# Kernel optimization log

Hardware: AMD Instinct MI355X
Metric: run time of the kernel (lower is better)

The kernel has to match this reference:

```python
import jax, jax.numpy as jnp
import numpy as np

N, E, IN, H, C = 50000, 800000, 128, 4, 32


def setup_inputs() -> dict:
    key = jax.random.key(0)
    ks = jax.random.split(key, 10)
    scale = 1.0 / np.sqrt(IN)
    x = jax.random.normal(ks[0], (N, IN), dtype=jnp.float32)
    edge_index = jax.random.randint(ks[1], (2, E), 0, N, dtype=jnp.int64)
    Wq = jax.random.uniform(ks[2], (IN, H * C), jnp.float32, -scale, scale)
    bq = jnp.zeros((H * C,), jnp.float32)
    Wk = jax.random.uniform(ks[3], (IN, H * C), jnp.float32, -scale, scale)
    bk = jnp.zeros((H * C,), jnp.float32)
    Wv = jax.random.uniform(ks[4], (IN, H * C), jnp.float32, -scale, scale)
    bv = jnp.zeros((H * C,), jnp.float32)
    Wskip = jax.random.uniform(ks[5], (IN, H * C), jnp.float32, -scale, scale)
    bskip = jnp.zeros((H * C,), jnp.float32)
    return {"x": x, "edge_index": edge_index, "Wq": Wq, "bq": bq,
            "Wk": Wk, "bk": bk, "Wv": Wv, "bv": bv,
            "Wskip": Wskip, "bskip": bskip}


def reference(x, edge_index, Wq, bq, Wk, bk, Wv, bv, Wskip, bskip):
    # PyG TransformerConv: edge messages flow src -> dst
    src, dst = edge_index[0], edge_index[1]
    q = (x @ Wq + bq).reshape(N, H, C)
    k = (x @ Wk + bk).reshape(N, H, C)
    v = (x @ Wv + bv).reshape(N, H, C)
    # per-edge attention logits [E, H]
    alpha = jnp.einsum('ehc,ehc->eh', q[dst], k[src]) / jnp.sqrt(jnp.float32(C))
    # scatter-softmax over incoming edges of each dst node
    m = jax.ops.segment_max(alpha, dst, num_segments=N)  # [N, H]
    ex = jnp.exp(alpha - m[dst])
    denom = jax.ops.segment_sum(ex, dst, num_segments=N)  # [N, H]
    w = ex / denom[dst]  # [E, H]
    # weighted scatter-add of values
    agg = jax.ops.segment_sum(v[src] * w[:, :, None], dst, num_segments=N)  # [N,H,C]
    out = agg.reshape(N, H * C) + x @ Wskip + bskip
    return out
```

## Files before the change

kernel.cpp:

```cpp
#include <hip/hip_runtime.h>
#include <hip/hip_bf16.h>

#define NNODES 50000
#define NEDGES 800000
#define FDIM   128
#define NHEADS 4
#define NSCANB ((NNODES + 1023) / 1024)

typedef __attribute__((ext_vector_type(8))) short  bf16x8;
typedef __attribute__((ext_vector_type(4))) float  f32x4;

static __device__ __forceinline__ unsigned short f2bf(float f) {
    __hip_bfloat16 h = __float2bfloat16(f);
    return *reinterpret_cast<unsigned short*>(&h);
}
static __device__ __forceinline__ float bf2f(unsigned short u) {
    return __uint_as_float(((unsigned int)u) << 16);
}

__global__ __launch_bounds__(256) void tgd_cvt_x(const float* __restrict__ x,
                                                 unsigned short* __restrict__ xb)
{
    size_t base = ((size_t)blockIdx.x * 256 + threadIdx.x) * 8;
    if (base >= (size_t)NNODES * FDIM) return;
    float4 f0 = *reinterpret_cast<const float4*>(&x[base]);
    float4 f1 = *reinterpret_cast<const float4*>(&x[base + 4]);
    unsigned short u[8];
    u[0]=f2bf(f0.x); u[1]=f2bf(f0.y); u[2]=f2bf(f0.z); u[3]=f2bf(f0.w);
    u[4]=f2bf(f1.x); u[5]=f2bf(f1.y); u[6]=f2bf(f1.z); u[7]=f2bf(f1.w);
    *reinterpret_cast<uint4*>(&xb[base]) = *reinterpret_cast<uint4*>(u);
}

__global__ __launch_bounds__(256) void tgd_cvt_w(
    const float* __restrict__ Wq, const float* __restrict__ Wk,
    const float* __restrict__ Wv, const float* __restrict__ Wsk,
    unsigned short* __restrict__ Wt2)
{
    int t = blockIdx.x * 256 + threadIdx.x;
    if (t >= 4 * 8 * 4 * 64) return;
    int m    = t >> 11;
    int ct   = (t >> 8) & 7;
    int ks   = (t >> 6) & 3;
    int lane = t & 63;
    int c  = ct * 16 + (lane & 15);
    int k0 = ks * 32 + (lane >> 4) * 8;
    const float* W = (m == 0) ? Wq : (m == 1) ? Wk : (m == 2) ? Wv : Wsk;
    unsigned short u[8];
    #pragma unroll
    for (int j = 0; j < 8; ++j)
        u[j] = f2bf(W[(size_t)(k0 + j) * FDIM + c]);
    *reinterpret_cast<uint4*>(&Wt2[(size_t)t * 8]) = *reinterpret_cast<uint4*>(u);
}

__global__ __launch_bounds__(512) void tgd_gemm_mfma(
    const unsigned short* __restrict__ xb, const unsigned short* __restrict__ Wt2,
    const float* __restrict__ bq, const float* __restrict__ bk,
    const float* __restrict__ bv, const float* __restrict__ bsk,
    float* __restrict__ q, unsigned short* __restrict__ kv,
    float* __restrict__ outp)
{
    const int tid  = threadIdx.x;
    const int wave = tid >> 6, lane = tid & 63;
    const int mp   = wave >> 2;
    const int wr   = wave & 3;
    const int r0   = blockIdx.x * 64 + wr * 16;
    const int l16  = lane & 15, lhi = lane >> 4;

    int arow = r0 + l16;
    int arow_c = (arow < NNODES) ? arow : (NNODES - 1);
    const unsigned short* abase = xb + (size_t)arow_c * FDIM + lhi * 8;
    bf16x8 a[4];
    #pragma unroll
    for (int ks = 0; ks < 4; ++ks)
        a[ks] = *reinterpret_cast<const bf16x8*>(abase + ks * 32);

    f32x4 acc[2][8];
    #pragma unroll
    for (int m2 = 0; m2 < 2; ++m2)
        #pragma unroll
        for (int ct = 0; ct < 8; ++ct)
            acc[m2][ct] = (f32x4){0.f, 0.f, 0.f, 0.f};

    #pragma unroll
    for (int ks = 0; ks < 4; ++ks) {
        #pragma unroll
        for (int m2 = 0; m2 < 2; ++m2) {
            const int m = mp * 2 + m2;
            const unsigned short* wb =
                Wt2 + ((size_t)(((m * 8 + 0) * 4 + ks) * 64) + lane) * 8;
            #pragma unroll
            for (int ct = 0; ct < 8; ++ct) {
                bf16x8 b = *reinterpret_cast<const bf16x8*>(wb + (size_t)ct * 4 * 64 * 8);
                acc[m2][ct] = __builtin_amdgcn_mfma_f32_16x16x32_bf16(
                    a[ks], b, acc[m2][ct], 0, 0, 0);
            }
        }
    }

    #pragma unroll
    for (int m2 = 0; m2 < 2; ++m2) {
        const int m = mp * 2 + m2;
        const float* bias = (m == 0) ? bq : (m == 1) ? bk : (m == 2) ? bv : bsk;
        #pragma unroll
        for (int ct = 0; ct < 8; ++ct) {
            int col = ct * 16 + l16;
            float bval = bias[col];
            #pragma unroll
            for (int r = 0; r < 4; ++r) {
                int row = r0 + lhi * 4 + r;
                if (row >= NNODES) continue;
                float val = acc[m2][ct][r] + bval;
                if (m == 0)       q[(size_t)row * FDIM + col] = val;
                else if (m == 3)  outp[(size_t)row * FDIM + col] = val;
                else              kv[(size_t)row * 256 + (m == 2 ? 128 : 0) + col] = f2bf(val);
            }
        }
    }
}

__global__ __launch_bounds__(256) void tgd_hist(const int* __restrict__ ei,
                                                int* __restrict__ deg)
{
    int t = blockIdx.x * 256 + threadIdx.x;
    if (t < NEDGES) atomicAdd(&deg[ei[NEDGES + t]], 1);
}

__global__ __launch_bounds__(1024) void tgd_scan1(const int* __restrict__ deg,
                                                  int* __restrict__ rowptr,
                                                  int* __restrict__ bsum)
{
    __shared__ int buf[1024];
    const int tid = threadIdx.x;
    const int i   = blockIdx.x * 1024 + tid;
    int d = (i < NNODES) ? deg[i] : 0;
    buf[tid] = d;
    __syncthreads();
    #pragma unroll
    for (int off = 1; off < 1024; off <<= 1) {
        int t2 = (tid >= off) ? buf[tid - off] : 0;
        __syncthreads();
        buf[tid] += t2;
        __syncthreads();
    }
    if (i < NNODES) rowptr[i + 1] = buf[tid];
    if (tid == 1023) bsum[blockIdx.x] = buf[1023];
}

__global__ __launch_bounds__(64) void tgd_scan2(const int* __restrict__ bsum,
                                                int* __restrict__ boff)
{
    int lane = threadIdx.x;
    int v = (lane < NSCANB) ? bsum[lane] : 0;
    int own = v;
    #pragma unroll
    for (int off = 1; off < 64; off <<= 1) {
        int t = __shfl_up(v, off);
        if (lane >= off) v += t;
    }
    if (lane < NSCANB) boff[lane] = v - own;
}

__global__ __launch_bounds__(1024) void tgd_scan3(const int* __restrict__ deg,
                                                  const int* __restrict__ boff,
                                                  int* __restrict__ rowptr,
                                                  int* __restrict__ ofs)
{
    const int i = blockIdx.x * 1024 + threadIdx.x;
    if (i < NNODES) {
        int r = rowptr[i + 1] + boff[blockIdx.x];
        rowptr[i + 1] = r;
        ofs[i] = r - deg[i];
    }
    if (i == 0) rowptr[0] = 0;
}

__global__ __launch_bounds__(256) void tgd_build(const int* __restrict__ ei,
                                                 int* __restrict__ ofs,
                                                 int* __restrict__ csr)
{
    int t = blockIdx.x * 256 + threadIdx.x;
    if (t >= NEDGES) return;
    int src = ei[t];
    int dst = ei[NEDGES + t];
    int pos = atomicAdd(&ofs[dst], 1);
    csr[pos] = src;
}

__global__ __launch_bounds__(256) void tgd_agg(
    const int* __restrict__ csr, const int* __restrict__ rowptr,
    const float* __restrict__ q, const unsigned short* __restrict__ kv,
    float* __restrict__ outp)
{
    const int node = blockIdx.x * 4 + (threadIdx.x >> 6);
    const int lane = threadIdx.x & 63;
    if (node >= NNODES) return;
    const int start = rowptr[node];
    const int end   = rowptr[node + 1];
    if (start == end) return;

    const bool isK = (lane < 32);
    float4 qv = {0.f, 0.f, 0.f, 0.f};
    if (isK) qv = *reinterpret_cast<const float4*>(&q[(size_t)node * FDIM + lane * 4]);
    const float inv = 0.17677669529663687f;

    float  den = 0.0f;
    float4 acc = {0.f, 0.f, 0.f, 0.f};

    for (int base = start; base < end; base += 64) {
        const int cnt = min(64, end - base);
        int myid = (lane < cnt) ? csr[base + lane] : 0;

        int j = 0;
        for (; j + 1 < cnt; j += 2) {
            int s0 = __shfl(myid, j);
            int s1 = __shfl(myid, j + 1);
            ushort4 r0 = *reinterpret_cast<const ushort4*>(&kv[(size_t)s0 * 256 + lane * 4]);
            ushort4 r1 = *reinterpret_cast<const ushort4*>(&kv[(size_t)s1 * 256 + lane * 4]);

            float a0 = bf2f(r0.x), a1 = bf2f(r0.y), a2 = bf2f(r0.z), a3 = bf2f(r0.w);
            float b0 = bf2f(r1.x), b1 = bf2f(r1.y), b2 = bf2f(r1.z), b3 = bf2f(r1.w);

            float sA = qv.x*a0 + qv.y*a1 + qv.z*a2 + qv.w*a3;
            float sB = qv.x*b0 + qv.y*b1 + qv.z*b2 + qv.w*b3;
            sA += __shfl_xor(sA, 1);  sB += __shfl_xor(sB, 1);
            sA += __shfl_xor(sA, 2);  sB += __shfl_xor(sB, 2);
            sA += __shfl_xor(sA, 4);  sB += __shfl_xor(sB, 4);
            float wA = __expf(sA * inv);
            float wB = __expf(sB * inv);
            wA = __shfl_xor(wA, 32);
            wB = __shfl_xor(wB, 32);
            if (!isK) {
                den += wA + wB;
                acc.x += wA*a0 + wB*b0;
                acc.y += wA*a1 + wB*b1;
                acc.z += wA*a2 + wB*b2;
                acc.w += wA*a3 + wB*b3;
            }
        }
        if (j < cnt) {
            int s0 = __shfl(myid, j);
            ushort4 r0 = *reinterpret_cast<const ushort4*>(&kv[(size_t)s0 * 256 + lane * 4]);
            float a0 = bf2f(r0.x), a1 = bf2f(r0.y), a2 = bf2f(r0.z), a3 = bf2f(r0.w);
            float sA = qv.x*a0 + qv.y*a1 + qv.z*a2 + qv.w*a3;
            sA += __shfl_xor(sA, 1);
            sA += __shfl_xor(sA, 2);
            sA += __shfl_xor(sA, 4);
            float wA = __expf(sA * inv);
            wA = __shfl_xor(wA, 32);
            if (!isK) {
                den += wA;
                acc.x += wA*a0; acc.y += wA*a1; acc.z += wA*a2; acc.w += wA*a3;
            }
        }
    }

    if (!isK) {
        float invd = 1.0f / den;
        float4* o = reinterpret_cast<float4*>(&outp[(size_t)node * FDIM + (lane - 32) * 4]);
        float4 cur = *o;
        cur.x += acc.x * invd;
        cur.y += acc.y * invd;
        cur.z += acc.z * invd;
        cur.w += acc.w * invd;
        *o = cur;
    }
}

extern "C" void kernel_launch(void* const* d_in, const int* in_sizes, int n_in,
                              void* d_out, int out_size, void* d_ws, size_t ws_size,
                              hipStream_t stream) {
    const float* x   = (const float*)d_in[0];
    const int*   ei  = (const int*)  d_in[1];
    const float* Wq  = (const float*)d_in[2];
    const float* bq  = (const float*)d_in[3];
    const float* Wk  = (const float*)d_in[4];
    const float* bk  = (const float*)d_in[5];
    const float* Wv  = (const float*)d_in[6];
    const float* bv  = (const float*)d_in[7];
    const float* Wsk = (const float*)d_in[8];
    const float* bsk = (const float*)d_in[9];
    float* outp = (float*)d_out;

    float* ws = (float*)d_ws;
    float*          q   = ws;
    unsigned short* kv  = (unsigned short*)(q + (size_t)NNODES * FDIM);
    unsigned short* xb  = kv + (size_t)NNODES * 256;
    unsigned short* Wt2 = xb + (size_t)NNODES * FDIM;
    int* deg    = (int*)(Wt2 + 4 * FDIM * FDIM);
    int* rowptr = deg + NNODES;
    int* ofs    = rowptr + NNODES + 1;
    int* csr    = ofs + NNODES;
    int* bsum   = csr + NEDGES;
    int* boff   = bsum + NSCANB;

    hipMemsetAsync(deg, 0, (size_t)NNODES * sizeof(int), stream);

    tgd_cvt_x<<<(NNODES * FDIM / 8 + 255) / 256, 256, 0, stream>>>(x, xb);
    tgd_cvt_w<<<(4 * 8 * 4 * 64 + 255) / 256, 256, 0, stream>>>(Wq, Wk, Wv, Wsk, Wt2);

    tgd_gemm_mfma<<<(NNODES + 63) / 64, 512, 0, stream>>>(
        xb, Wt2, bq, bk, bv, bsk, q, kv, outp);

    tgd_hist<<<(NEDGES + 255) / 256, 256, 0, stream>>>(ei, deg);
    tgd_scan1<<<NSCANB, 1024, 0, stream>>>(deg, rowptr, bsum);
    tgd_scan2<<<1, 64, 0, stream>>>(bsum, boff);
    tgd_scan3<<<NSCANB, 1024, 0, stream>>>(deg, boff, rowptr, ofs);
    tgd_build<<<(NEDGES + 255) / 256, 256, 0, stream>>>(ei, ofs, csr);
    tgd_agg<<<(NNODES + 3) / 4, 256, 0, stream>>>(csr, rowptr, q, kv, outp);
}
```

Before: 334.2 us.

## Pre-tile x into MFMA fragment layout and stage GEMM outputs through LDS

The x conversion kernel now writes bf16 data directly in the per-lane MFMA A-fragment order, zero-padding tail rows, so each GEMM wave loads its fragments with fully contiguous reads. The GEMM epilogue stages q, the skip output and the packed k/v tile through a 32KB shared buffer, then writes rows with coalesced float4/uint4 stores instead of scattered scalar stores. The cost is extra LDS use, several block barriers and the strided reads from x in the conversion kernel.

```diff
diff --git a/kernel.cpp b/kernel.cpp
--- a/kernel.cpp
+++ b/kernel.cpp
@@ -6,6 +6,8 @@
 #define FDIM   128
 #define NHEADS 4
 #define NSCANB ((NNODES + 1023) / 1024)
+#define NBLK   782
+#define NT16   (NBLK * 4)
 
 typedef __attribute__((ext_vector_type(8))) short  bf16x8;
 typedef __attribute__((ext_vector_type(4))) float  f32x4;
@@ -18,17 +20,27 @@
     return __uint_as_float(((unsigned int)u) << 16);
 }
 
-__global__ __launch_bounds__(256) void tgd_cvt_x(const float* __restrict__ x,
-                                                 unsigned short* __restrict__ xb)
-{
-    size_t base = ((size_t)blockIdx.x * 256 + threadIdx.x) * 8;
-    if (base >= (size_t)NNODES * FDIM) return;
-    float4 f0 = *reinterpret_cast<const float4*>(&x[base]);
-    float4 f1 = *reinterpret_cast<const float4*>(&x[base + 4]);
+__global__ __launch_bounds__(256) void tgd_cvt_xa(const float* __restrict__ x,
+                                                  unsigned short* __restrict__ xa)
+{
+    int t = blockIdx.x * 256 + threadIdx.x;
+    if (t >= NT16 * 4 * 64) return;
+    int lane = t & 63;
+    int ks   = (t >> 6) & 3;
+    int gt   = t >> 8;
+    int row  = gt * 16 + (lane & 15);
+    int k0   = ks * 32 + (lane >> 4) * 8;
     unsigned short u[8];
-    u[0]=f2bf(f0.x); u[1]=f2bf(f0.y); u[2]=f2bf(f0.z); u[3]=f2bf(f0.w);
-    u[4]=f2bf(f1.x); u[5]=f2bf(f1.y); u[6]=f2bf(f1.z); u[7]=f2bf(f1.w);
-    *reinterpret_cast<uint4*>(&xb[base]) = *reinterpret_cast<uint4*>(u);
+    if (row < NNODES) {
+        float4 f0 = *reinterpret_cast<const float4*>(&x[(size_t)row * FDIM + k0]);
+        float4 f1 = *reinterpret_cast<const float4*>(&x[(size_t)row * FDIM + k0 + 4]);
+        u[0]=f2bf(f0.x); u[1]=f2bf(f0.y); u[2]=f2bf(f0.z); u[3]=f2bf(f0.w);
+        u[4]=f2bf(f1.x); u[5]=f2bf(f1.y); u[6]=f2bf(f1.z); u[7]=f2bf(f1.w);
+    } else {
+        #pragma unroll
+        for (int j = 0; j < 8; ++j) u[j] = 0;
+    }
+    *reinterpret_cast<uint4*>(&xa[(size_t)t * 8]) = *reinterpret_cast<uint4*>(u);
 }
 
 __global__ __launch_bounds__(256) void tgd_cvt_w(
@@ -53,26 +65,28 @@
 }
 
 __global__ __launch_bounds__(512) void tgd_gemm_mfma(
-    const unsigned short* __restrict__ xb, const unsigned short* __restrict__ Wt2,
+    const unsigned short* __restrict__ xa, const unsigned short* __restrict__ Wt2,
     const float* __restrict__ bq, const float* __restrict__ bk,
     const float* __restrict__ bv, const float* __restrict__ bsk,
     float* __restrict__ q, unsigned short* __restrict__ kv,
     float* __restrict__ outp)
 {
+    __shared__ float st[64 * 128];
+    unsigned short* sth = (unsigned short*)st;
+
     const int tid  = threadIdx.x;
     const int wave = tid >> 6, lane = tid & 63;
     const int mp   = wave >> 2;
     const int wr   = wave & 3;
-    const int r0   = blockIdx.x * 64 + wr * 16;
     const int l16  = lane & 15, lhi = lane >> 4;
-
-    int arow = r0 + l16;
-    int arow_c = (arow < NNODES) ? arow : (NNODES - 1);
-    const unsigned short* abase = xb + (size_t)arow_c * FDIM + lhi * 8;
+    const int gt   = blockIdx.x * 4 + wr;
+    const int base = blockIdx.x * 64;
+
     bf16x8 a[4];
     #pragma unroll
     for (int ks = 0; ks < 4; ++ks)
-        a[ks] = *reinterpret_cast<const bf16x8*>(abase + ks * 32);
+        a[ks] = *reinterpret_cast<const bf16x8*>(
+            xa + ((size_t)(gt * 4 + ks) * 64 + lane) * 8);
 
     f32x4 acc[2][8];
     #pragma unroll
@@ -87,34 +101,81 @@
         for (int m2 = 0; m2 < 2; ++m2) {
             const int m = mp * 2 + m2;
             const unsigned short* wb =
-                Wt2 + ((size_t)(((m * 8 + 0) * 4 + ks) * 64) + lane) * 8;
+                Wt2 + ((size_t)((m * 8 * 4 + ks) * 64) + lane) * 8;
             #pragma unroll
             for (int ct = 0; ct < 8; ++ct) {
-                bf16x8 b = *reinterpret_cast<const bf16x8*>(wb + (size_t)ct * 4 * 64 * 8);
+                bf16x8 b = *reinterpret_cast<const bf16x8*>(wb + (size_t)ct * 2048);
                 acc[m2][ct] = __builtin_amdgcn_mfma_f32_16x16x32_bf16(
                     a[ks], b, acc[m2][ct], 0, 0, 0);
             }
         }
     }
 
-    #pragma unroll
-    for (int m2 = 0; m2 < 2; ++m2) {
-        const int m = mp * 2 + m2;
-        const float* bias = (m == 0) ? bq : (m == 1) ? bk : (m == 2) ? bv : bsk;
+    const int rowl0 = wr * 16 + lhi * 4;
+
+    if (mp == 0) {
+        #pragma unroll
+        for (int ct = 0; ct < 8; ++ct) {
+            int col = ct * 16 + l16;
+            float bval = bq[col];
+            #pragma unroll
+            for (int r = 0; r < 4; ++r)
+                st[(rowl0 + r) * 128 + col] = acc[0][ct][r] + bval;
+        }
+    }
+    __syncthreads();
+    #pragma unroll
+    for (int i = 0; i < 4; ++i) {
+        int idx = i * 512 + tid;
+        int row = idx >> 5, c4 = idx & 31;
+        if (base + row < NNODES)
+            *reinterpret_cast<float4*>(&q[(size_t)(base + row) * FDIM + c4 * 4]) =
+                *reinterpret_cast<const float4*>(&st[row * 128 + c4 * 4]);
+    }
+    __syncthreads();
+
+    if (mp == 1) {
+        #pragma unroll
+        for (int ct = 0; ct < 8; ++ct) {
+            int col = ct * 16 + l16;
+            float bval = bsk[col];
+            #pragma unroll
+            for (int r = 0; r < 4; ++r)
+                st[(rowl0 + r) * 128 + col] = acc[1][ct][r] + bval;
+        }
+    }
+    __syncthreads();
+    #pragma unroll
+    for (int i = 0; i < 4; ++i) {
+        int idx = i * 512 + tid;
+        int row = idx >> 5, c4 = idx & 31;
+        if (base + row < NNODES)
+            *reinterpret_cast<float4*>(&outp[(size_t)(base + row) * FDIM + c4 * 4]) =
+                *reinterpret_cast<const float4*>(&st[row * 128 + c4 * 4]);
+    }
+    __syncthreads();
+
+    {
+        const int off  = (mp == 0) ? 0 : 128;
+        const int m2s  = (mp == 0) ? 1 : 0;
+        const float* bias = (mp == 0) ? bk : bv;
         #pragma unroll
         for (int ct = 0; ct < 8; ++ct) {
             int col = ct * 16 + l16;
             float bval = bias[col];
             #pragma unroll
-            for (int r = 0; r < 4; ++r) {
-                int row = r0 + lhi * 4 + r;
-                if (row >= NNODES) continue;
-                float val = acc[m2][ct][r] + bval;
-                if (m == 0)       q[(size_t)row * FDIM + col] = val;
-                else if (m == 3)  outp[(size_t)row * FDIM + col] = val;
-                else              kv[(size_t)row * 256 + (m == 2 ? 128 : 0) + col] = f2bf(val);
-            }
-        }
+            for (int r = 0; r < 4; ++r)
+                sth[(rowl0 + r) * 256 + off + col] = f2bf(acc[m2s][ct][r] + bval);
+        }
+    }
+    __syncthreads();
+    #pragma unroll
+    for (int i = 0; i < 4; ++i) {
+        int idx = i * 512 + tid;
+        int row = idx >> 5, c8 = idx & 31;
+        if (base + row < NNODES)
+            *reinterpret_cast<uint4*>(&kv[(size_t)(base + row) * 256 + c8 * 8]) =
+                *reinterpret_cast<const uint4*>(&sth[row * 256 + c8 * 8]);
     }
 }
 
@@ -284,8 +345,8 @@
     float* ws = (float*)d_ws;
     float*          q   = ws;
     unsigned short* kv  = (unsigned short*)(q + (size_t)NNODES * FDIM);
-    unsigned short* xb  = kv + (size_t)NNODES * 256;
-    unsigned short* Wt2 = xb + (size_t)NNODES * FDIM;
+    unsigned short* xa  = kv + (size_t)NNODES * 256;
+    unsigned short* Wt2 = xa + (size_t)NT16 * 4 * 64 * 8;
     int* deg    = (int*)(Wt2 + 4 * FDIM * FDIM);
     int* rowptr = deg + NNODES;
     int* ofs    = rowptr + NNODES + 1;
@@ -295,11 +356,11 @@
 
     hipMemsetAsync(deg, 0, (size_t)NNODES * sizeof(int), stream);
 
-    tgd_cvt_x<<<(NNODES * FDIM / 8 + 255) / 256, 256, 0, stream>>>(x, xb);
+    tgd_cvt_xa<<<(NT16 * 4 * 64 + 255) / 256, 256, 0, stream>>>(x, xa);
     tgd_cvt_w<<<(4 * 8 * 4 * 64 + 255) / 256, 256, 0, stream>>>(Wq, Wk, Wv, Wsk, Wt2);
 
-    tgd_gemm_mfma<<<(NNODES + 63) / 64, 512, 0, stream>>>(
-        xb, Wt2, bq, bk, bv, bsk, q, kv, outp);
+    tgd_gemm_mfma<<<NBLK, 512, 0, stream>>>(
+        xa, Wt2, bq, bk, bv, bsk, q, kv, outp);
 
     tgd_hist<<<(NEDGES + 255) / 256, 256, 0, stream>>>(ei, deg);
     tgd_scan1<<<NSCANB, 1024, 0, stream>>>(deg, rowptr, bsum);
```

After: 310.4 us. 1.08x faster.
